# Kernel tuning notes

Hardware: AMD Instinct MI355X
Metric: run time of the kernel (lower is better)

The kernel has to match this reference:

```python
import jax, jax.numpy as jnp
import numpy as np

B, L, D, H = 4, 2048, 1024, 16
HD = D // H  # head_dim = 64


def setup_inputs() -> dict:
    key = jax.random.key(0)
    k1, k2, k3 = jax.random.split(key, 3)
    scale_in = 1.0 / np.sqrt(D)
    return {
        "x": jax.random.normal(k1, (B, L, D), dtype=jnp.float32),
        "Wqkv": jax.random.normal(k2, (D, 3 * D), dtype=jnp.float32) * scale_in,
        "Wout": jax.random.normal(k3, (D, D), dtype=jnp.float32) * scale_in,
        "bout": jnp.zeros((D,), dtype=jnp.float32),
    }


def reference(x, Wqkv, Wout, bout):
    b, l, d = x.shape
    # QKV projection (no bias): [B, L, 3D] -> [B, L, 3, H, HD]
    qkv = (x @ Wqkv).reshape(b, l, 3, H, HD)
    q, k, v = jnp.moveaxis(qkv, 2, 0)  # each [B, L, H, HD]
    # scaled scores [B, H, L, L]
    scores = jnp.einsum("blhd,bmhd->bhlm", q, k) / jnp.sqrt(jnp.float32(HD))
    causal_mask = jnp.triu(jnp.ones((l, l), dtype=bool), k=1)
    scores = jnp.where(causal_mask, -jnp.inf, scores)
    attn = jax.nn.softmax(scores, axis=-1)
    # dropout p=0.0 (eval-mode reference) -> identity
    out = jnp.einsum("bhlm,bmhd->blhd", attn, v).reshape(b, l, d)
    return out @ Wout + bout
```

## Files before the change

### kernel.cpp

```cpp
#include <hip/hip_runtime.h>

typedef unsigned short ushort_t;
using bf16x8 = __attribute__((ext_vector_type(8))) short;
using f32x4  = __attribute__((ext_vector_type(4))) float;
using f32x16 = __attribute__((ext_vector_type(16))) float;
using u32x4  = __attribute__((ext_vector_type(4))) unsigned int;

#define B_  4
#define L_  2048
#define D_  1024
#define H_  16
#define HD_ 64
#define N3_ 3072
#define M1_ (B_ * L_)

static __device__ __forceinline__ unsigned short f2bf(float f) {
    unsigned int u = __float_as_uint(f);
    unsigned int r = (u + 0x7fffu + ((u >> 16) & 1u)) >> 16;
    return (unsigned short)r;
}

static __device__ __forceinline__ unsigned int pkbf(float lo, float hi) {
    unsigned int r;
    asm("v_cvt_pk_bf16_f32 %0, %1, %2" : "=v"(r) : "v"(lo), "v"(hi));
    return r;
}

static __device__ __forceinline__ void plswap(unsigned int& a, unsigned int& b) {
    asm volatile("v_permlane32_swap_b32 %0, %1" : "+v"(a), "+v"(b));
}

static __device__ __forceinline__ void async16(const void* g, const void* l) {
    __builtin_amdgcn_global_load_lds(
        (const __attribute__((address_space(1))) void*)g,
        (__attribute__((address_space(3))) void*)l, 16, 0, 0);
}

__global__ void convert_x_kernel(const float4* __restrict__ src,
                                 ushort4* __restrict__ dst) {
    int i = blockIdx.x * blockDim.x + threadIdx.x;
    float4 v = src[i];
    ushort4 o;
    o.x = f2bf(v.x); o.y = f2bf(v.y); o.z = f2bf(v.z); o.w = f2bf(v.w);
    dst[i] = o;
}

__global__ void transpose_conv_kernel(const float* __restrict__ src,
                                      unsigned short* __restrict__ dst,
                                      int rows, int cols) {
    __shared__ float tile[32][33];
    int tx = threadIdx.x, ty = threadIdx.y;
    int c0 = blockIdx.x * 32, r0 = blockIdx.y * 32;
    #pragma unroll
    for (int j = 0; j < 32; j += 8)
        tile[ty + j][tx] = src[(size_t)(r0 + ty + j) * cols + c0 + tx];
    __syncthreads();
    #pragma unroll
    for (int j = 0; j < 32; j += 8)
        dst[(size_t)(c0 + ty + j) * rows + r0 + tx] = f2bf(tile[tx][ty + j]);
}

template <int EPI>
__global__ __launch_bounds__(256) void gemm_bt_kernel(
    const unsigned short* __restrict__ A, const unsigned short* __restrict__ BT,
    unsigned short* __restrict__ qb, unsigned short* __restrict__ kb,
    unsigned short* __restrict__ vtb, float* __restrict__ outp,
    const float* __restrict__ bias) {
    constexpr int K = 1024;
    __shared__ unsigned short As[128 * 32];
    __shared__ unsigned short Bs[128 * 32];
    const int tid = threadIdx.x, w = tid >> 6, lane = tid & 63;
    const int m0 = blockIdx.y * 128, n0 = blockIdx.x * 128;
    const int wm = (w >> 1) * 64, wn = (w & 1) * 64;
    const int lg = lane >> 4, ll = lane & 15;

    f32x4 acc[4][4] = {};

    for (int k0 = 0; k0 < K; k0 += 32) {
        #pragma unroll
        for (int j = 0; j < 2; ++j) {
            int row = w * 32 + j * 16 + (lane >> 2);
            int col = (lane & 3) * 8;
            async16(&A[(size_t)(m0 + row) * K + k0 + col], &As[(w * 32 + j * 16) * 32]);
            async16(&BT[(size_t)(n0 + row) * K + k0 + col], &Bs[(w * 32 + j * 16) * 32]);
        }
        __syncthreads();
        bf16x8 af[4], bfr[4];
        #pragma unroll
        for (int i = 0; i < 4; ++i) {
            af[i]  = *(const bf16x8*)&As[(wm + i * 16 + ll) * 32 + lg * 8];
            bfr[i] = *(const bf16x8*)&Bs[(wn + i * 16 + ll) * 32 + lg * 8];
        }
        #pragma unroll
        for (int mi = 0; mi < 4; ++mi)
            #pragma unroll
            for (int ni = 0; ni < 4; ++ni)
                acc[mi][ni] = __builtin_amdgcn_mfma_f32_16x16x32_bf16(
                    af[mi], bfr[ni], acc[mi][ni], 0, 0, 0);
        __syncthreads();
    }

    #pragma unroll
    for (int mi = 0; mi < 4; ++mi)
        #pragma unroll
        for (int ni = 0; ni < 4; ++ni)
            #pragma unroll
            for (int r = 0; r < 4; ++r) {
                int m = m0 + wm + mi * 16 + lg * 4 + r;
                int n = n0 + wn + ni * 16 + ll;
                float v = acc[mi][ni][r];
                if (EPI == 0) {
                    int b = m >> 11, l = m & 2047;
                    int s = n >> 10, h = (n >> 6) & 15, hd = n & 63;
                    int bh = b * H_ + h;
                    unsigned short bv = f2bf(v);
                    size_t base = (size_t)bh * (L_ * HD_);
                    if (s == 2) {
                        vtb[base + (l >> 5) * 2048 + ((l >> 4) & 1) * 1024 +
                            ((l >> 3) & 1) * 512 + hd * 8 + (l & 7)] = bv;
                    } else {
                        size_t o = base + (l >> 5) * 2048 + (hd >> 4) * 512 +
                                   ((hd >> 3) & 1) * 256 + (l & 31) * 8 + (hd & 7);
                        if (s == 0) qb[o] = bv; else kb[o] = bv;
                    }
                } else {
                    outp[(size_t)m * D_ + n] = v + bias[n];
                }
            }
}

__global__ __launch_bounds__(256) void attn_kernel(
    const unsigned short* __restrict__ qbuf, const unsigned short* __restrict__ kbuf,
    const unsigned short* __restrict__ vbuf, unsigned short* __restrict__ obuf) {
    __shared__ float Sden[4][32];

    const int tid = threadIdx.x;
    const int w = tid >> 6, lane = tid & 63;
    const int lq = lane & 31;
    const int hi = lane >> 5;

    const int bid = blockIdx.x;
    const int grp = bid >> 6;
    const int bh  = bid & 63;
    const int qt  = (15 - grp) * 4 + w;
    const int q0  = qt * 32;

    const unsigned short* Qf = qbuf + (size_t)bh * (L_ * HD_);
    const unsigned short* Kf = kbuf + (size_t)bh * (L_ * HD_);
    const unsigned short* Vf = vbuf + (size_t)bh * (L_ * HD_);

    bf16x8 qf[4];
    #pragma unroll
    for (int c = 0; c < 4; ++c)
        qf[c] = *(const bf16x8*)&Qf[qt * 2048 + c * 512 + hi * 256 + lq * 8];

    f32x16 oa0 = {}, oa1 = {};
    float sden = 0.f;

    const float C1 = 0.18033688011112042f;
    const float C2 = 7.2134752044448165f;

    const int ntiles = qt + 1;

    bf16x8 kf[4];
    #pragma unroll
    for (int c = 0; c < 4; ++c)
        kf[c] = *(const bf16x8*)&Kf[c * 512 + hi * 256 + lq * 8];

    for (int t = 0; t < ntiles; ++t) {
        bf16x8 v0f[2], v1f[2];
        #pragma unroll
        for (int c = 0; c < 2; ++c) {
            v0f[c] = *(const bf16x8*)&Vf[t * 2048 + c * 1024 + hi * 512 + lq * 8];
            v1f[c] = *(const bf16x8*)&Vf[t * 2048 + c * 1024 + hi * 512 + 256 + lq * 8];
        }
        bf16x8 nk[4];
        const bool more = (t + 1 < ntiles);
        if (more) {
            #pragma unroll
            for (int c = 0; c < 4; ++c)
                nk[c] = *(const bf16x8*)&Kf[(t + 1) * 2048 + c * 512 + hi * 256 + lq * 8];
        }

        f32x16 st = {};
        __builtin_amdgcn_s_setprio(1);
        #pragma unroll
        for (int c = 0; c < 4; ++c)
            st = __builtin_amdgcn_mfma_f32_32x32x16_bf16(kf[c], qf[c], st, 0, 0, 0);
        __builtin_amdgcn_s_setprio(0);

        float p[16];
        float rs = 0.f;
        const bool diag = (t == qt);
        #pragma unroll
        for (int r = 0; r < 16; ++r) {
            float pv = exp2f(fmaf(st[r], C1, -C2));
            if (diag) {
                int kv = (r & 3) + 8 * (r >> 2) + 4 * hi;
                if (kv > lq) pv = 0.f;
            }
            p[r] = pv;
            rs += pv;
        }
        rs += __shfl_xor(rs, 32);
        sden += rs;

        unsigned int a0 = pkbf(p[0],  p[1]),  a1 = pkbf(p[2],  p[3]);
        unsigned int b0 = pkbf(p[4],  p[5]),  b1 = pkbf(p[6],  p[7]);
        unsigned int c0 = pkbf(p[8],  p[9]),  c1 = pkbf(p[10], p[11]);
        unsigned int d0 = pkbf(p[12], p[13]), d1 = pkbf(p[14], p[15]);
        plswap(a0, b0);
        plswap(a1, b1);
        plswap(c0, d0);
        plswap(c1, d1);
        u32x4 t0 = {a0, a1, b0, b1};
        u32x4 t1 = {c0, c1, d0, d1};
        bf16x8 pa0 = __builtin_bit_cast(bf16x8, t0);
        bf16x8 pa1 = __builtin_bit_cast(bf16x8, t1);

        __builtin_amdgcn_s_setprio(1);
        oa0 = __builtin_amdgcn_mfma_f32_32x32x16_bf16(pa0, v0f[0], oa0, 0, 0, 0);
        oa1 = __builtin_amdgcn_mfma_f32_32x32x16_bf16(pa0, v1f[0], oa1, 0, 0, 0);
        oa0 = __builtin_amdgcn_mfma_f32_32x32x16_bf16(pa1, v0f[1], oa0, 0, 0, 0);
        oa1 = __builtin_amdgcn_mfma_f32_32x32x16_bf16(pa1, v1f[1], oa1, 0, 0, 0);
        __builtin_amdgcn_s_setprio(0);

        if (more) {
            #pragma unroll
            for (int c = 0; c < 4; ++c) kf[c] = nk[c];
        }
    }

    if (hi == 0) Sden[w][lq] = 1.0f / sden;
    __builtin_amdgcn_s_waitcnt(0);

    const int b = bh >> 4, h = bh & 15;
    #pragma unroll
    for (int r = 0; r < 16; ++r) {
        int q = (r & 3) + 8 * (r >> 2) + 4 * hi;
        float inv = Sden[w][q];
        float o0 = oa0[r] * inv;
        float o1 = oa1[r] * inv;
        size_t row = (size_t)(b * L_ + q0 + q) * D_ + h * HD_;
        obuf[row + lq]      = f2bf(o0);
        obuf[row + 32 + lq] = f2bf(o1);
    }
}

extern "C" void kernel_launch(void* const* d_in, const int* in_sizes, int n_in,
                              void* d_out, int out_size, void* d_ws, size_t ws_size,
                              hipStream_t stream) {
    const float* x    = (const float*)d_in[0];
    const float* Wqkv = (const float*)d_in[1];
    const float* Wout = (const float*)d_in[2];
    const float* bout = (const float*)d_in[3];
    float* out = (float*)d_out;

    char* ws = (char*)d_ws;
    size_t off = 0;
    unsigned short* xb     = (unsigned short*)(ws + off); off += (size_t)M1_ * D_ * 2;
    unsigned short* wqkvT  = (unsigned short*)(ws + off); off += (size_t)N3_ * D_ * 2;
    unsigned short* woutT  = (unsigned short*)(ws + off); off += (size_t)D_ * D_ * 2;
    unsigned short* qb     = (unsigned short*)(ws + off); off += (size_t)B_ * H_ * L_ * HD_ * 2;
    unsigned short* kb     = (unsigned short*)(ws + off); off += (size_t)B_ * H_ * L_ * HD_ * 2;
    unsigned short* vb     = (unsigned short*)(ws + off); off += (size_t)B_ * H_ * L_ * HD_ * 2;
    unsigned short* attnb  = (unsigned short*)(ws + off); off += (size_t)M1_ * D_ * 2;

    convert_x_kernel<<<(M1_ * D_ / 4) / 256, 256, 0, stream>>>(
        (const float4*)x, (ushort4*)xb);
    transpose_conv_kernel<<<dim3(N3_ / 32, D_ / 32), dim3(32, 8), 0, stream>>>(
        Wqkv, wqkvT, D_, N3_);
    transpose_conv_kernel<<<dim3(D_ / 32, D_ / 32), dim3(32, 8), 0, stream>>>(
        Wout, woutT, D_, D_);

    gemm_bt_kernel<0><<<dim3(N3_ / 128, M1_ / 128), 256, 0, stream>>>(
        xb, wqkvT, qb, kb, vb, nullptr, nullptr);

    attn_kernel<<<dim3(16 * 64), 256, 0, stream>>>(qb, kb, vb, attnb);

    gemm_bt_kernel<1><<<dim3(D_ / 128, M1_ / 128), 256, 0, stream>>>(
        attnb, woutT, nullptr, nullptr, nullptr, out, bout);
}
```

Before: 201.1 us.

## Use 256x256-tile, 4-stage pipelined GEMM for the QKV projection

Replaces the 128x128 QKV projection GEMM with a dedicated 512-thread kernel. It uses 256x256 tiles, a 4-deep async LDS ring buffer with explicit vmcnt waits, a workgroup-id swizzle for L2 locality, and s_setprio around the MFMA block. The V-transpose epilogue now writes packed ushort4 stores. Together these aim for more operand reuse and better overlap of global loads with MFMAs. In exchange the kernel has a much larger LDS footprint (128 KB per block) and fewer workgroups (384), so occupancy and tail effects could hurt.

Result: faster. 188.3 us (-6.4%).

```diff
diff --git a/kernel.cpp b/kernel.cpp
--- a/kernel.cpp
+++ b/kernel.cpp
@@ -60,12 +60,113 @@
         dst[(size_t)(c0 + ty + j) * rows + r0 + tx] = f2bf(tile[tx][ty + j]);
 }
 
-template <int EPI>
+__global__ __launch_bounds__(512, 2) void gemm256_qkv_kernel(
+    const unsigned short* __restrict__ A, const unsigned short* __restrict__ BT,
+    unsigned short* __restrict__ qb, unsigned short* __restrict__ kb,
+    unsigned short* __restrict__ vb) {
+    constexpr int K = 1024, BK = 32, NT = K / BK;
+    constexpr int NBX = N3_ / 256;
+    constexpr int NWG = (M1_ / 256) * NBX;
+    __shared__ __align__(16) unsigned short lds[4][2][256 * BK];
+
+    const int tid = threadIdx.x;
+    const int w = tid >> 6, lane = tid & 63;
+    const int wr = w >> 2, wc = w & 3;
+    const int lg = lane >> 4, ll = lane & 15;
+
+    const int bid = blockIdx.x;
+    const int swz = (bid & 7) * (NWG / 8) + (bid >> 3);
+    const int m0 = (swz / NBX) * 256, n0 = (swz % NBX) * 256;
+
+    const int srow = w * 16 + (lane >> 2);
+    const int scol = (lane & 3) * 8;
+
+    f32x4 acc[8][4] = {};
+
+    #pragma unroll 1
+    for (int kt = -3; kt < NT; ++kt) {
+        const int ks = kt + 3;
+        if (ks < NT) {
+            const int buf = ks & 3;
+            const size_t koff = (size_t)ks * BK + scol;
+            #pragma unroll
+            for (int rd = 0; rd < 2; ++rd) {
+                async16(&A[(size_t)(m0 + rd * 128 + srow) * K + koff],
+                        &lds[buf][0][w * 512 + rd * 4096]);
+                async16(&BT[(size_t)(n0 + rd * 128 + srow) * K + koff],
+                        &lds[buf][1][w * 512 + rd * 4096]);
+            }
+        }
+        if (kt < 0) continue;
+
+        if (kt == 0) {
+            asm volatile("s_waitcnt vmcnt(12)" ::: "memory");
+        } else if (kt <= NT - 4) {
+            asm volatile("s_waitcnt vmcnt(8)" ::: "memory");
+        } else if (kt == NT - 3) {
+            asm volatile("s_waitcnt vmcnt(4)" ::: "memory");
+        } else {
+            asm volatile("s_waitcnt vmcnt(0)" ::: "memory");
+        }
+        __builtin_amdgcn_s_barrier();
+        __builtin_amdgcn_sched_barrier(0);
+
+        const unsigned short* Ab = &lds[kt & 3][0][0];
+        const unsigned short* Bb = &lds[kt & 3][1][0];
+        bf16x8 af[8], bf[4];
+        #pragma unroll
+        for (int i = 0; i < 8; ++i)
+            af[i] = *(const bf16x8*)&Ab[(wr * 128 + i * 16 + ll) * BK + lg * 8];
+        #pragma unroll
+        for (int j = 0; j < 4; ++j)
+            bf[j] = *(const bf16x8*)&Bb[(wc * 64 + j * 16 + ll) * BK + lg * 8];
+
+        __builtin_amdgcn_s_setprio(1);
+        #pragma unroll
+        for (int i = 0; i < 8; ++i)
+            #pragma unroll
+            for (int j = 0; j < 4; ++j)
+                acc[i][j] = __builtin_amdgcn_mfma_f32_16x16x32_bf16(
+                    af[i], bf[j], acc[i][j], 0, 0, 0);
+        __builtin_amdgcn_s_setprio(0);
+    }
+
+    #pragma unroll
+    for (int mi = 0; mi < 8; ++mi) {
+        const int mb = m0 + wr * 128 + mi * 16 + lg * 4;
+        #pragma unroll
+        for (int ni = 0; ni < 4; ++ni) {
+            const int n = n0 + wc * 64 + ni * 16 + ll;
+            const int s = n >> 10, h = (n >> 6) & 15, hd = n & 63;
+            if (s == 2) {
+                const int b = mb >> 11, l = mb & 2047;
+                const size_t base = (size_t)(b * H_ + h) * (L_ * HD_);
+                ushort4 pk;
+                pk.x = f2bf(acc[mi][ni][0]);
+                pk.y = f2bf(acc[mi][ni][1]);
+                pk.z = f2bf(acc[mi][ni][2]);
+                pk.w = f2bf(acc[mi][ni][3]);
+                *(ushort4*)&vb[base + (l >> 5) * 2048 + ((l >> 4) & 1) * 1024 +
+                               ((l >> 3) & 1) * 512 + hd * 8 + (l & 7)] = pk;
+            } else {
+                #pragma unroll
+                for (int r = 0; r < 4; ++r) {
+                    const int m = mb + r;
+                    const int b = m >> 11, l = m & 2047;
+                    const size_t base = (size_t)(b * H_ + h) * (L_ * HD_);
+                    const size_t o = base + (l >> 5) * 2048 + (hd >> 4) * 512 +
+                                     ((hd >> 3) & 1) * 256 + (l & 31) * 8 + (hd & 7);
+                    unsigned short bv = f2bf(acc[mi][ni][r]);
+                    if (s == 0) qb[o] = bv; else kb[o] = bv;
+                }
+            }
+        }
+    }
+}
+
 __global__ __launch_bounds__(256) void gemm_bt_kernel(
     const unsigned short* __restrict__ A, const unsigned short* __restrict__ BT,
-    unsigned short* __restrict__ qb, unsigned short* __restrict__ kb,
-    unsigned short* __restrict__ vtb, float* __restrict__ outp,
-    const float* __restrict__ bias) {
+    float* __restrict__ outp, const float* __restrict__ bias) {
     constexpr int K = 1024;
     __shared__ unsigned short As[128 * 32];
     __shared__ unsigned short Bs[128 * 32];
@@ -108,24 +209,7 @@
             for (int r = 0; r < 4; ++r) {
                 int m = m0 + wm + mi * 16 + lg * 4 + r;
                 int n = n0 + wn + ni * 16 + ll;
-                float v = acc[mi][ni][r];
-                if (EPI == 0) {
-                    int b = m >> 11, l = m & 2047;
-                    int s = n >> 10, h = (n >> 6) & 15, hd = n & 63;
-                    int bh = b * H_ + h;
-                    unsigned short bv = f2bf(v);
-                    size_t base = (size_t)bh * (L_ * HD_);
-                    if (s == 2) {
-                        vtb[base + (l >> 5) * 2048 + ((l >> 4) & 1) * 1024 +
-                            ((l >> 3) & 1) * 512 + hd * 8 + (l & 7)] = bv;
-                    } else {
-                        size_t o = base + (l >> 5) * 2048 + (hd >> 4) * 512 +
-                                   ((hd >> 3) & 1) * 256 + (l & 31) * 8 + (hd & 7);
-                        if (s == 0) qb[o] = bv; else kb[o] = bv;
-                    }
-                } else {
-                    outp[(size_t)m * D_ + n] = v + bias[n];
-                }
+                outp[(size_t)m * D_ + n] = acc[mi][ni][r] + bias[n];
             }
 }
 
@@ -273,11 +357,11 @@
     transpose_conv_kernel<<<dim3(D_ / 32, D_ / 32), dim3(32, 8), 0, stream>>>(
         Wout, woutT, D_, D_);
 
-    gemm_bt_kernel<0><<<dim3(N3_ / 128, M1_ / 128), 256, 0, stream>>>(
-        xb, wqkvT, qb, kb, vb, nullptr, nullptr);
+    gemm256_qkv_kernel<<<dim3((M1_ / 256) * (N3_ / 256)), 512, 0, stream>>>(
+        xb, wqkvT, qb, kb, vb);
 
     attn_kernel<<<dim3(16 * 64), 256, 0, stream>>>(qb, kb, vb, attnb);
 
-    gemm_bt_kernel<1><<<dim3(D_ / 128, M1_ / 128), 256, 0, stream>>>(
-        attnb, woutT, nullptr, nullptr, nullptr, out, bout);
-}
+    gemm_bt_kernel<<<dim3(D_ / 128, M1_ / 128), 256, 0, stream>>>(
+        attnb, woutT, out, bout);
+}
```
